# Kernel optimization log

Hardware: AMD Instinct MI355X
Metric: run time of the kernel (lower is better)

Reference implementation:

```python
import math
import jax, jax.numpy as jnp
import numpy as np

SQRT_2_OVER_PI = 0.7978845608028654
FACIL_RATE = 2.0
FIRE_THRESH = 0.88
EPS = 1e-05

def _gelu(x):
    return 0.5 * x * (1.0 + jnp.tanh(SQRT_2_OVER_PI * (x + 0.044715 * x ** 3)))

def setup_inputs() -> dict:
    key = jax.random.key(0)
    ks = jax.random.split(key, 8)
    B, T, D, N = 4, 4096, 1024, 512
    x = jax.random.normal(ks[0], (B, T, D), jnp.float32)
    ema_x = jax.random.normal(ks[1], (D,), jnp.float32) * 0.1
    ema_x2 = ema_x ** 2 + jax.random.uniform(ks[2], (D,), jnp.float32) + 0.5
    ema_y = jax.random.normal(ks[3], (D,), jnp.float32) * 0.1
    ema_y2 = ema_y ** 2 + jax.random.uniform(ks[4], (D,), jnp.float32) + 0.5
    buf = jax.random.normal(ks[5], (N, D), jnp.float32)
    buf = buf / jnp.linalg.norm(buf, axis=-1, keepdims=True)
    facil = 1.0 + 2.0 * jax.random.uniform(ks[6], (N,), jnp.float32)  # facilitation levels >= 1
    mask = jnp.ones((N,), dtype=bool)
    return {
        'x': x,
        'log_tau_in': jnp.float32(math.log(1.0)),
        'log_tau_out': jnp.float32(math.log(1.0)),
        'log_a_in': jnp.float32(0.0),
        'log_a_out': jnp.float32(0.0),
        'log_k_boost': jnp.float32(math.log(0.5)),
        'log_k_damp': jnp.float32(math.log(0.3)),
        'ema_x': ema_x, 'ema_x2': ema_x2, 'ema_y': ema_y, 'ema_y2': ema_y2,
        'buf': buf, 'facil': facil, 'mask': mask,
    }

def reference(x, log_tau_in, log_tau_out, log_a_in, log_a_out,
              log_k_boost, log_k_damp, ema_x, ema_x2, ema_y, ema_y2,
              buf, facil, mask):
    sg = jax.lax.stop_gradient
    D = x.shape[-1]
    y = _gelu(x)
    # --- gate_211 (l1_ready steady state); z-statistics are detached in torch ---
    tau_in, tau_out = jnp.exp(log_tau_in), jnp.exp(log_tau_out)
    a_in, a_out = jax.nn.sigmoid(log_a_in), jax.nn.sigmoid(log_a_out)
    std_x = jnp.sqrt(jnp.clip(sg(ema_x2) - sg(ema_x) ** 2, 0.0)) + EPS
    z_in = jnp.mean(((sg(x) - sg(ema_x)) / std_x) ** 2, axis=-1)        # [B,T]
    std_y = jnp.sqrt(jnp.clip(sg(ema_y2) - sg(ema_y) ** 2, 0.0)) + EPS
    z_out = jnp.mean(((sg(y) - sg(ema_y)) / std_y) ** 2, axis=-1)       # [B,T]
    g_in = 1.0 - a_in + a_in * jnp.exp(-tau_in * z_in)
    g_out = 1.0 - a_out + a_out * jnp.exp(-tau_out * z_out)
    gate = g_in * g_out
    y1 = y * gate[..., None]
    # --- eval-time OCS nearest-neighbor facilitation (l2_ready, pass1_complete) ---
    k_boost = jnp.clip(jnp.exp(log_k_boost), 0.01, 4.0)
    k_damp = jnp.clip(jnp.exp(log_k_damp), 0.01, 0.9)
    y1_mean = jnp.mean(sg(y1).reshape(-1, D), axis=0)                    # [D]
    m_n = y1_mean / jnp.maximum(jnp.linalg.norm(y1_mean), 1e-12)
    buf_sg = sg(buf)
    buf_n = buf_sg / jnp.maximum(jnp.linalg.norm(buf_sg, axis=-1, keepdims=True), 1e-12)
    sims = jnp.where(mask, buf_n @ m_n, -1.0)                            # [N]
    nearest_idx = jnp.argmax(sims)
    sim_val = jnp.clip(sims[nearest_idx], 0.0, 1.0)
    fired = sim_val > FIRE_THRESH
    facil_level = sg(facil)[nearest_idx] * jnp.where(fired, FACIL_RATE, 1.0)
    v = buf_sg[nearest_idx]                                              # [D]
    valid = jnp.all(jnp.isfinite(v)) & (jnp.linalg.norm(v) >= 1e-06)
    mod = (facil_level - 1.0) * sim_val
    boost = 1.0 + sg(k_boost) * mod            # torch uses .item(): detached
    damp = jnp.maximum(0.01, 1.0 - sg(k_damp) * mod)
    proj = jnp.sum(y1 * v, axis=-1, keepdims=True)
    y_par = proj * v
    out = jnp.where(valid, y_par * boost + (y1 - y_par) * damp, y1)
    return out
```

## Files before the change

kernel.cpp:

```cpp
#include <hip/hip_runtime.h>
#include <math.h>

#define D 1024
#define NROWS 16384
#define NBUF 512
#define NBLKA 512
#define NSLOT 512

#define OFF_MEAN 0
#define OFF_KEY  1024
#define OFF_GATE 2048
#define OFF_PART 20480
#define ZERO_BYTES 4112

typedef float nfloat4 __attribute__((ext_vector_type(4)));

__device__ __forceinline__ float4 ld4(const float* p) { return *(const float4*)p; }
__device__ __forceinline__ void st4_nt(float* p, float4 v) {
    nfloat4 nv = { v.x, v.y, v.z, v.w };
    __builtin_nontemporal_store(nv, (nfloat4*)p);
}

__device__ __forceinline__ float wave_red(float v) {
    #pragma unroll
    for (int off = 32; off > 0; off >>= 1) v += __shfl_xor(v, off, 64);
    return v;
}

__device__ __forceinline__ float gelu_f(float x) {
    float x2 = x * x;
    float t1 = fmaf(0.044715f, x2, 1.0f);
    float u2 = (1.5957691216057308f * x) * t1;
    float e  = __expf(u2);
    float r  = __builtin_amdgcn_rcpf(e + 1.0f);
    return fmaf(-x, r, x);
}

__device__ __forceinline__ float4 gelu4(float4 x) {
    float4 y;
    y.x = gelu_f(x.x); y.y = gelu_f(x.y); y.z = gelu_f(x.z); y.w = gelu_f(x.w);
    return y;
}

#define LOADPAIR(rr, XA, XB) do {                                              \
    const float* _pA = x + (size_t)(rr) * D;                                   \
    const float* _pB = _pA + D;                                                \
    _Pragma("unroll")                                                          \
    for (int _j = 0; _j < 4; ++_j) {                                           \
        XA[_j] = ld4(&_pA[col[_j]]);                                           \
        XB[_j] = ld4(&_pB[col[_j]]);                                           \
    }                                                                          \
} while (0)

__global__ __launch_bounds__(256, 2) void k_passA(const float* __restrict__ x,
                                                  const float* __restrict__ ema_x,
                                                  const float* __restrict__ ema_x2,
                                                  const float* __restrict__ ema_y,
                                                  const float* __restrict__ ema_y2,
                                                  const float* __restrict__ lti,
                                                  const float* __restrict__ lto,
                                                  const float* __restrict__ lai,
                                                  const float* __restrict__ lao,
                                                  float* __restrict__ ws) {
    __shared__ float s_stat[4096];
    __shared__ float s_acc[D];
    const int tid = threadIdx.x, wave = tid >> 6, lane = tid & 63;

    for (int i = tid; i < 1024; i += 256) {
        float mx = ema_x[i];
        float vx = fmaxf(ema_x2[i] - mx * mx, 0.0f);
        float ax = 1.0f / (sqrtf(vx) + 1e-5f);
        s_stat[i]        = ax;
        s_stat[1024 + i] = mx * ax;
        float my = ema_y[i];
        float vy = fmaxf(ema_y2[i] - my * my, 0.0f);
        float ay = 1.0f / (sqrtf(vy) + 1e-5f);
        s_stat[2048 + i] = ay;
        s_stat[3072 + i] = my * ay;
        s_acc[i] = 0.0f;
    }
    __syncthreads();

    const float tau_in = __expf(lti[0]), tau_out = __expf(lto[0]);
    const float a_in  = 1.0f / (1.0f + __expf(-lai[0]));
    const float a_out = 1.0f / (1.0f + __expf(-lao[0]));

    int col[4];
    #pragma unroll
    for (int j = 0; j < 4; ++j) col[j] = 4 * lane + 256 * j;

    float4 acc[4];
    #pragma unroll
    for (int j = 0; j < 4; ++j) acc[j] = make_float4(0.f, 0.f, 0.f, 0.f);

#define COMPPAIR_A(rr, XA, XB) do {                                            \
    float4 yA[4], yB[4];                                                       \
    float zinA = 0.f, zinB = 0.f, zoutA = 0.f, zoutB = 0.f;                    \
    _Pragma("unroll")                                                          \
    for (int j = 0; j < 4; ++j) {                                              \
        float4 a  = *(const float4*)&s_stat[col[j]];                           \
        float4 bb = *(const float4*)&s_stat[1024 + col[j]];                    \
        float d;                                                               \
        d = fmaf(XA[j].x, a.x, -bb.x); zinA = fmaf(d, d, zinA);                \
        d = fmaf(XA[j].y, a.y, -bb.y); zinA = fmaf(d, d, zinA);                \
        d = fmaf(XA[j].z, a.z, -bb.z); zinA = fmaf(d, d, zinA);                \
        d = fmaf(XA[j].w, a.w, -bb.w); zinA = fmaf(d, d, zinA);                \
        d = fmaf(XB[j].x, a.x, -bb.x); zinB = fmaf(d, d, zinB);                \
        d = fmaf(XB[j].y, a.y, -bb.y); zinB = fmaf(d, d, zinB);                \
        d = fmaf(XB[j].z, a.z, -bb.z); zinB = fmaf(d, d, zinB);                \
        d = fmaf(XB[j].w, a.w, -bb.w); zinB = fmaf(d, d, zinB);                \
        yA[j] = gelu4(XA[j]);                                                  \
        yB[j] = gelu4(XB[j]);                                                  \
        float4 ay = *(const float4*)&s_stat[2048 + col[j]];                    \
        float4 by = *(const float4*)&s_stat[3072 + col[j]];                    \
        d = fmaf(yA[j].x, ay.x, -by.x); zoutA = fmaf(d, d, zoutA);             \
        d = fmaf(yA[j].y, ay.y, -by.y); zoutA = fmaf(d, d, zoutA);             \
        d = fmaf(yA[j].z, ay.z, -by.z); zoutA = fmaf(d, d, zoutA);             \
        d = fmaf(yA[j].w, ay.w, -by.w); zoutA = fmaf(d, d, zoutA);             \
        d = fmaf(yB[j].x, ay.x, -by.x); zoutB = fmaf(d, d, zoutB);             \
        d = fmaf(yB[j].y, ay.y, -by.y); zoutB = fmaf(d, d, zoutB);             \
        d = fmaf(yB[j].z, ay.z, -by.z); zoutB = fmaf(d, d, zoutB);             \
        d = fmaf(yB[j].w, ay.w, -by.w); zoutB = fmaf(d, d, zoutB);             \
    }                                                                          \
    zinA  = wave_red(zinA)  * (1.0f / D);                                      \
    zinB  = wave_red(zinB)  * (1.0f / D);                                      \
    zoutA = wave_red(zoutA) * (1.0f / D);                                      \
    zoutB = wave_red(zoutB) * (1.0f / D);                                      \
    float gA = ((1.0f - a_in)  + a_in  * __expf(-tau_in  * zinA)) *            \
               ((1.0f - a_out) + a_out * __expf(-tau_out * zoutA));            \
    float gB = ((1.0f - a_in)  + a_in  * __expf(-tau_in  * zinB)) *            \
               ((1.0f - a_out) + a_out * __expf(-tau_out * zoutB));            \
    if (lane == 0) { ws[OFF_GATE + (rr)] = gA; ws[OFF_GATE + (rr) + 1] = gB; } \
    _Pragma("unroll")                                                          \
    for (int j = 0; j < 4; ++j) {                                              \
        acc[j].x = fmaf(yA[j].x, gA, fmaf(yB[j].x, gB, acc[j].x));             \
        acc[j].y = fmaf(yA[j].y, gA, fmaf(yB[j].y, gB, acc[j].y));             \
        acc[j].z = fmaf(yA[j].z, gA, fmaf(yB[j].z, gB, acc[j].z));             \
        acc[j].w = fmaf(yA[j].w, gA, fmaf(yB[j].w, gB, acc[j].w));             \
    }                                                                          \
} while (0)

    const int r0 = (blockIdx.x * 4 + wave) * 8;
    float4 xA0[4], xB0[4], xA1[4], xB1[4];

    LOADPAIR(r0 + 0, xA0, xB0);
    LOADPAIR(r0 + 2, xA1, xB1);
    COMPPAIR_A(r0 + 0, xA0, xB0);
    LOADPAIR(r0 + 4, xA0, xB0);
    COMPPAIR_A(r0 + 2, xA1, xB1);
    LOADPAIR(r0 + 6, xA1, xB1);
    COMPPAIR_A(r0 + 4, xA0, xB0);
    COMPPAIR_A(r0 + 6, xA1, xB1);

    #pragma unroll
    for (int j = 0; j < 4; ++j) {
        atomicAdd(&s_acc[col[j] + 0], acc[j].x);
        atomicAdd(&s_acc[col[j] + 1], acc[j].y);
        atomicAdd(&s_acc[col[j] + 2], acc[j].z);
        atomicAdd(&s_acc[col[j] + 3], acc[j].w);
    }
    __syncthreads();
    *(float4*)&ws[OFF_PART + (size_t)blockIdx.x * D + 4 * tid] = *(float4*)&s_acc[4 * tid];
}

__global__ __launch_bounds__(256) void k_mean(float* __restrict__ ws) {
    const int tid = threadIdx.x;
    const float* P = &ws[OFF_PART + (size_t)blockIdx.x * 16 * D];
    float4 s = make_float4(0.f, 0.f, 0.f, 0.f);
    #pragma unroll
    for (int i = 0; i < 16; ++i) {
        float4 v = ld4(&P[(size_t)i * D + 4 * tid]);
        s.x += v.x; s.y += v.y; s.z += v.z; s.w += v.w;
    }
    atomicAdd(&ws[OFF_MEAN + 4 * tid + 0], s.x);
    atomicAdd(&ws[OFF_MEAN + 4 * tid + 1], s.y);
    atomicAdd(&ws[OFF_MEAN + 4 * tid + 2], s.z);
    atomicAdd(&ws[OFF_MEAN + 4 * tid + 3], s.w);
}

__global__ __launch_bounds__(256) void k_sims(const float* __restrict__ buf,
                                              const unsigned char* __restrict__ mask,
                                              float* __restrict__ ws) {
    __shared__ float s_red[4];
    __shared__ float s_inv;
    const int tid = threadIdx.x, wave = tid >> 6, lane = tid & 63;

    float4 mv = ld4(&ws[OFF_MEAN + 4 * tid]);
    float ns = mv.x * mv.x + mv.y * mv.y + mv.z * mv.z + mv.w * mv.w;
    ns = wave_red(ns);
    if (lane == 0) s_red[wave] = ns;
    __syncthreads();
    if (tid == 0) {
        float t = s_red[0] + s_red[1] + s_red[2] + s_red[3];
        s_inv = 1.0f / fmaxf(sqrtf(t), 1e-12f);
    }
    __syncthreads();
    const float inv = s_inv;

    int col[4];
    float4 mvv[4];
    #pragma unroll
    for (int j = 0; j < 4; ++j) {
        col[j] = 4 * lane + 256 * j;
        mvv[j] = ld4(&ws[OFF_MEAN + col[j]]);
    }
    const int n = blockIdx.x * 4 + wave;
    const float* br = buf + (size_t)n * D;
    float dot = 0.f, bns = 0.f;
    #pragma unroll
    for (int j = 0; j < 4; ++j) {
        float4 bv = ld4(&br[col[j]]);
        dot = fmaf(bv.x, mvv[j].x, dot); dot = fmaf(bv.y, mvv[j].y, dot);
        dot = fmaf(bv.z, mvv[j].z, dot); dot = fmaf(bv.w, mvv[j].w, dot);
        bns = fmaf(bv.x, bv.x, bns); bns = fmaf(bv.y, bv.y, bns);
        bns = fmaf(bv.z, bv.z, bns); bns = fmaf(bv.w, bv.w, bns);
    }
    dot = wave_red(dot);
    bns = wave_red(bns);
    if (lane == 0) {
        float sim = -1.0f;
        if (mask[n]) sim = (dot * inv) / fmaxf(sqrtf(bns), 1e-12f);
        unsigned int fb = __float_as_uint(sim);
        unsigned int mono = (fb & 0x80000000u) ? ~fb : (fb | 0x80000000u);
        unsigned long long key = ((unsigned long long)mono << 32) | (unsigned int)(~n);
        atomicMax((unsigned long long*)&ws[OFF_KEY], key);
    }
}

__global__ __launch_bounds__(256, 2) void k_passB(const float* __restrict__ x,
                                                  const float* __restrict__ buf,
                                                  const float* __restrict__ facil,
                                                  const float* __restrict__ lkb,
                                                  const float* __restrict__ lkd,
                                                  const float* __restrict__ ws,
                                                  float* __restrict__ out) {
    __shared__ float s_v[D];
    __shared__ float s_red[4];
    __shared__ float s_sc[3];
    const int tid = threadIdx.x, wave = tid >> 6, lane = tid & 63;

    const unsigned long long key = *(const unsigned long long*)&ws[OFF_KEY];
    const int idx = (int)(~(unsigned int)(key & 0xFFFFFFFFull));
    const unsigned int mono = (unsigned int)(key >> 32);
    const unsigned int fb = (mono & 0x80000000u) ? (mono ^ 0x80000000u) : ~mono;
    const float sim = __uint_as_float(fb);

    float4 vt = ld4(&buf[(size_t)idx * D + 4 * tid]);
    float bns = 0.f;
    if (!isfinite(vt.x) || !isfinite(vt.y) || !isfinite(vt.z) || !isfinite(vt.w))
        bns = __uint_as_float(0x7FC00000u);
    bns += vt.x * vt.x + vt.y * vt.y + vt.z * vt.z + vt.w * vt.w;
    bns = wave_red(bns);
    if (lane == 0) s_red[wave] = bns;
    __syncthreads();
    if (tid == 0) {
        float t = s_red[0] + s_red[1] + s_red[2] + s_red[3];
        int valid = (t >= 1e-12f) ? 1 : 0;
        float sim_val = fminf(fmaxf(sim, 0.0f), 1.0f);
        float fl = facil[idx] * ((sim_val > 0.88f) ? 2.0f : 1.0f);
        float mod = (fl - 1.0f) * sim_val;
        float kb = fminf(fmaxf(__expf(lkb[0]), 0.01f), 4.0f);
        float kd = fminf(fmaxf(__expf(lkd[0]), 0.01f), 0.9f);
        float boost = 1.0f + kb * mod;
        float damp = fmaxf(0.01f, 1.0f - kd * mod);
        s_sc[0] = valid ? damp : 1.0f;
        s_sc[1] = valid ? (boost - damp) : 0.0f;
        s_sc[2] = (float)valid;
    }
    __syncthreads();
    const float dampe = s_sc[0], coef = s_sc[1];
    if (s_sc[2] == 0.0f) vt = make_float4(0.f, 0.f, 0.f, 0.f);
    *(float4*)&s_v[4 * tid] = vt;
    __syncthreads();

    int col[4];
    float4 vv[4];
    #pragma unroll
    for (int j = 0; j < 4; ++j) {
        col[j] = 4 * lane + 256 * j;
        vv[j] = *(const float4*)&s_v[col[j]];
    }

#define COMPPAIR_B(rr, XA, XB) do {                                            \
    const float gA = ws[OFF_GATE + (rr)], gB = ws[OFF_GATE + (rr) + 1];        \
    float4 yA[4], yB[4];                                                       \
    float projA = 0.f, projB = 0.f;                                            \
    _Pragma("unroll")                                                          \
    for (int j = 0; j < 4; ++j) {                                              \
        yA[j] = gelu4(XA[j]);                                                  \
        yA[j].x *= gA; yA[j].y *= gA; yA[j].z *= gA; yA[j].w *= gA;            \
        yB[j] = gelu4(XB[j]);                                                  \
        yB[j].x *= gB; yB[j].y *= gB; yB[j].z *= gB; yB[j].w *= gB;            \
        projA = fmaf(yA[j].x, vv[j].x, projA); projA = fmaf(yA[j].y, vv[j].y, projA); \
        projA = fmaf(yA[j].z, vv[j].z, projA); projA = fmaf(yA[j].w, vv[j].w, projA); \
        projB = fmaf(yB[j].x, vv[j].x, projB); projB = fmaf(yB[j].y, vv[j].y, projB); \
        projB = fmaf(yB[j].z, vv[j].z, projB); projB = fmaf(yB[j].w, vv[j].w, projB); \
    }                                                                          \
    projA = wave_red(projA);                                                   \
    projB = wave_red(projB);                                                   \
    const float pcA = projA * coef, pcB = projB * coef;                        \
    float* oA = out + (size_t)(rr) * D;                                        \
    float* oB = oA + D;                                                        \
    _Pragma("unroll")                                                          \
    for (int j = 0; j < 4; ++j) {                                              \
        float4 o;                                                              \
        o.x = fmaf(yA[j].x, dampe, pcA * vv[j].x);                             \
        o.y = fmaf(yA[j].y, dampe, pcA * vv[j].y);                             \
        o.z = fmaf(yA[j].z, dampe, pcA * vv[j].z);                             \
        o.w = fmaf(yA[j].w, dampe, pcA * vv[j].w);                             \
        st4_nt(&oA[col[j]], o);                                                \
        o.x = fmaf(yB[j].x, dampe, pcB * vv[j].x);                             \
        o.y = fmaf(yB[j].y, dampe, pcB * vv[j].y);                             \
        o.z = fmaf(yB[j].z, dampe, pcB * vv[j].z);                             \
        o.w = fmaf(yB[j].w, dampe, pcB * vv[j].w);                             \
        st4_nt(&oB[col[j]], o);                                                \
    }                                                                          \
} while (0)

    const int r0 = (blockIdx.x * 4 + wave) * 8;
    float4 xA0[4], xB0[4], xA1[4], xB1[4];

    LOADPAIR(r0 + 0, xA0, xB0);
    LOADPAIR(r0 + 2, xA1, xB1);
    COMPPAIR_B(r0 + 0, xA0, xB0);
    LOADPAIR(r0 + 4, xA0, xB0);
    COMPPAIR_B(r0 + 2, xA1, xB1);
    LOADPAIR(r0 + 6, xA1, xB1);
    COMPPAIR_B(r0 + 4, xA0, xB0);
    COMPPAIR_B(r0 + 6, xA1, xB1);
}

extern "C" void kernel_launch(void* const* d_in, const int* in_sizes, int n_in,
                              void* d_out, int out_size, void* d_ws, size_t ws_size,
                              hipStream_t stream) {
    const float* x      = (const float*)d_in[0];
    const float* lti    = (const float*)d_in[1];
    const float* lto    = (const float*)d_in[2];
    const float* lai    = (const float*)d_in[3];
    const float* lao    = (const float*)d_in[4];
    const float* lkb    = (const float*)d_in[5];
    const float* lkd    = (const float*)d_in[6];
    const float* ema_x  = (const float*)d_in[7];
    const float* ema_x2 = (const float*)d_in[8];
    const float* ema_y  = (const float*)d_in[9];
    const float* ema_y2 = (const float*)d_in[10];
    const float* buf    = (const float*)d_in[11];
    const float* facil  = (const float*)d_in[12];
    const unsigned char* mask = (const unsigned char*)d_in[13];
    float* ws  = (float*)d_ws;
    float* out = (float*)d_out;

    (void)hipMemsetAsync(d_ws, 0, ZERO_BYTES, stream);
    hipLaunchKernelGGL(k_passA, dim3(NBLKA), dim3(256), 0, stream,
                       x, ema_x, ema_x2, ema_y, ema_y2, lti, lto, lai, lao, ws);
    hipLaunchKernelGGL(k_mean,  dim3(NSLOT / 16), dim3(256), 0, stream, ws);
    hipLaunchKernelGGL(k_sims,  dim3(128), dim3(256), 0, stream, buf, mask, ws);
    hipLaunchKernelGGL(k_passB, dim3(NBLKA), dim3(256), 0, stream,
                       x, buf, facil, lkb, lkd, ws, out);
}
```

Measured before the change: 176.5 us.

## Fuse all passes into one cooperative kernel keeping gated activations in registers

```diff
diff --git a/kernel.cpp b/kernel.cpp
--- a/kernel.cpp
+++ b/kernel.cpp
@@ -1,10 +1,13 @@
 #include <hip/hip_runtime.h>
+#include <hip/hip_cooperative_groups.h>
 #include <math.h>
+
+namespace cg = cooperative_groups;
 
 #define D 1024
 #define NROWS 16384
 #define NBUF 512
-#define NBLKA 512
+#define NBLK 512
 #define NSLOT 512
 
 #define OFF_MEAN 0
@@ -51,6 +54,247 @@
         XB[_j] = ld4(&_pB[col[_j]]);                                           \
     }                                                                          \
 } while (0)
+
+__global__ __launch_bounds__(256, 2) void k_fused(
+    const float* __restrict__ x,
+    const float* __restrict__ ema_x,  const float* __restrict__ ema_x2,
+    const float* __restrict__ ema_y,  const float* __restrict__ ema_y2,
+    const float* __restrict__ lti,    const float* __restrict__ lto,
+    const float* __restrict__ lai,    const float* __restrict__ lao,
+    const float* __restrict__ lkb,    const float* __restrict__ lkd,
+    const float* __restrict__ buf,    const float* __restrict__ facil,
+    const unsigned char* __restrict__ mask,
+    float* __restrict__ ws,           float* __restrict__ out)
+{
+    cg::grid_group grid = cg::this_grid();
+    __shared__ float s_stat[4096];
+    __shared__ float s_acc[D];
+    __shared__ float s_red[4];
+    __shared__ float s_sc[3];
+    __shared__ float s_inv;
+    const int tid = threadIdx.x, wave = tid >> 6, lane = tid & 63;
+
+    for (int i = tid; i < 1024; i += 256) {
+        float mx = ema_x[i];
+        float vx = fmaxf(ema_x2[i] - mx * mx, 0.0f);
+        float ax = 1.0f / (sqrtf(vx) + 1e-5f);
+        s_stat[i]        = ax;
+        s_stat[1024 + i] = mx * ax;
+        float my = ema_y[i];
+        float vy = fmaxf(ema_y2[i] - my * my, 0.0f);
+        float ay = 1.0f / (sqrtf(vy) + 1e-5f);
+        s_stat[2048 + i] = ay;
+        s_stat[3072 + i] = my * ay;
+        s_acc[i] = 0.0f;
+    }
+    __syncthreads();
+
+    const float tau_in = __expf(lti[0]), tau_out = __expf(lto[0]);
+    const float a_in  = 1.0f / (1.0f + __expf(-lai[0]));
+    const float a_out = 1.0f / (1.0f + __expf(-lao[0]));
+
+    int col[4];
+    #pragma unroll
+    for (int j = 0; j < 4; ++j) col[j] = 4 * lane + 256 * j;
+
+    float4 acc[4];
+    #pragma unroll
+    for (int j = 0; j < 4; ++j) acc[j] = make_float4(0.f, 0.f, 0.f, 0.f);
+
+#define COMPPAIR_F(XA, XB, YA, YB) do {                                        \
+    float zinA = 0.f, zinB = 0.f, zoutA = 0.f, zoutB = 0.f;                    \
+    _Pragma("unroll")                                                          \
+    for (int j = 0; j < 4; ++j) {                                              \
+        float4 a  = *(const float4*)&s_stat[col[j]];                           \
+        float4 bb = *(const float4*)&s_stat[1024 + col[j]];                    \
+        float d;                                                               \
+        d = fmaf(XA[j].x, a.x, -bb.x); zinA = fmaf(d, d, zinA);                \
+        d = fmaf(XA[j].y, a.y, -bb.y); zinA = fmaf(d, d, zinA);                \
+        d = fmaf(XA[j].z, a.z, -bb.z); zinA = fmaf(d, d, zinA);                \
+        d = fmaf(XA[j].w, a.w, -bb.w); zinA = fmaf(d, d, zinA);                \
+        d = fmaf(XB[j].x, a.x, -bb.x); zinB = fmaf(d, d, zinB);                \
+        d = fmaf(XB[j].y, a.y, -bb.y); zinB = fmaf(d, d, zinB);                \
+        d = fmaf(XB[j].z, a.z, -bb.z); zinB = fmaf(d, d, zinB);                \
+        d = fmaf(XB[j].w, a.w, -bb.w); zinB = fmaf(d, d, zinB);                \
+        YA[j] = gelu4(XA[j]);                                                  \
+        YB[j] = gelu4(XB[j]);                                                  \
+        float4 ay = *(const float4*)&s_stat[2048 + col[j]];                    \
+        float4 by = *(const float4*)&s_stat[3072 + col[j]];                    \
+        d = fmaf(YA[j].x, ay.x, -by.x); zoutA = fmaf(d, d, zoutA);             \
+        d = fmaf(YA[j].y, ay.y, -by.y); zoutA = fmaf(d, d, zoutA);             \
+        d = fmaf(YA[j].z, ay.z, -by.z); zoutA = fmaf(d, d, zoutA);             \
+        d = fmaf(YA[j].w, ay.w, -by.w); zoutA = fmaf(d, d, zoutA);             \
+        d = fmaf(YB[j].x, ay.x, -by.x); zoutB = fmaf(d, d, zoutB);             \
+        d = fmaf(YB[j].y, ay.y, -by.y); zoutB = fmaf(d, d, zoutB);             \
+        d = fmaf(YB[j].z, ay.z, -by.z); zoutB = fmaf(d, d, zoutB);             \
+        d = fmaf(YB[j].w, ay.w, -by.w); zoutB = fmaf(d, d, zoutB);             \
+    }                                                                          \
+    zinA  = wave_red(zinA)  * (1.0f / D);                                      \
+    zinB  = wave_red(zinB)  * (1.0f / D);                                      \
+    zoutA = wave_red(zoutA) * (1.0f / D);                                      \
+    zoutB = wave_red(zoutB) * (1.0f / D);                                      \
+    float gA = ((1.0f - a_in)  + a_in  * __expf(-tau_in  * zinA)) *            \
+               ((1.0f - a_out) + a_out * __expf(-tau_out * zoutA));            \
+    float gB = ((1.0f - a_in)  + a_in  * __expf(-tau_in  * zinB)) *            \
+               ((1.0f - a_out) + a_out * __expf(-tau_out * zoutB));            \
+    _Pragma("unroll")                                                          \
+    for (int j = 0; j < 4; ++j) {                                              \
+        YA[j].x *= gA; YA[j].y *= gA; YA[j].z *= gA; YA[j].w *= gA;            \
+        YB[j].x *= gB; YB[j].y *= gB; YB[j].z *= gB; YB[j].w *= gB;            \
+        acc[j].x += YA[j].x + YB[j].x;                                         \
+        acc[j].y += YA[j].y + YB[j].y;                                         \
+        acc[j].z += YA[j].z + YB[j].z;                                         \
+        acc[j].w += YA[j].w + YB[j].w;                                         \
+    }                                                                          \
+} while (0)
+
+    const int r0 = (blockIdx.x * 4 + wave) * 8;
+    float4 xA0[4], xB0[4], xA1[4], xB1[4];
+    float4 y0A[4], y0B[4], y1A[4], y1B[4], y2A[4], y2B[4], y3A[4], y3B[4];
+
+    LOADPAIR(r0 + 0, xA0, xB0);
+    LOADPAIR(r0 + 2, xA1, xB1);
+    COMPPAIR_F(xA0, xB0, y0A, y0B);
+    LOADPAIR(r0 + 4, xA0, xB0);
+    COMPPAIR_F(xA1, xB1, y1A, y1B);
+    LOADPAIR(r0 + 6, xA1, xB1);
+    COMPPAIR_F(xA0, xB0, y2A, y2B);
+    COMPPAIR_F(xA1, xB1, y3A, y3B);
+#undef COMPPAIR_F
+
+    #pragma unroll
+    for (int j = 0; j < 4; ++j) {
+        atomicAdd(&s_acc[col[j] + 0], acc[j].x);
+        atomicAdd(&s_acc[col[j] + 1], acc[j].y);
+        atomicAdd(&s_acc[col[j] + 2], acc[j].z);
+        atomicAdd(&s_acc[col[j] + 3], acc[j].w);
+    }
+    __syncthreads();
+    {
+        float4 a4 = *(float4*)&s_acc[4 * tid];
+        atomicAdd(&ws[OFF_MEAN + 4 * tid + 0], a4.x);
+        atomicAdd(&ws[OFF_MEAN + 4 * tid + 1], a4.y);
+        atomicAdd(&ws[OFF_MEAN + 4 * tid + 2], a4.z);
+        atomicAdd(&ws[OFF_MEAN + 4 * tid + 3], a4.w);
+    }
+
+    grid.sync();
+
+    if (blockIdx.x < NBUF / 4) {
+        float4 mv = ld4(&ws[OFF_MEAN + 4 * tid]);
+        float ns = mv.x * mv.x + mv.y * mv.y + mv.z * mv.z + mv.w * mv.w;
+        ns = wave_red(ns);
+        if (lane == 0) s_red[wave] = ns;
+        __syncthreads();
+        if (tid == 0) {
+            float t = s_red[0] + s_red[1] + s_red[2] + s_red[3];
+            s_inv = 1.0f / fmaxf(sqrtf(t), 1e-12f);
+        }
+        __syncthreads();
+        const float inv = s_inv;
+
+        float4 mvv[4];
+        #pragma unroll
+        for (int j = 0; j < 4; ++j) mvv[j] = ld4(&ws[OFF_MEAN + col[j]]);
+        const int n = blockIdx.x * 4 + wave;
+        const float* br = buf + (size_t)n * D;
+        float dot = 0.f, bns = 0.f;
+        #pragma unroll
+        for (int j = 0; j < 4; ++j) {
+            float4 bv = ld4(&br[col[j]]);
+            dot = fmaf(bv.x, mvv[j].x, dot); dot = fmaf(bv.y, mvv[j].y, dot);
+            dot = fmaf(bv.z, mvv[j].z, dot); dot = fmaf(bv.w, mvv[j].w, dot);
+            bns = fmaf(bv.x, bv.x, bns); bns = fmaf(bv.y, bv.y, bns);
+            bns = fmaf(bv.z, bv.z, bns); bns = fmaf(bv.w, bv.w, bns);
+        }
+        dot = wave_red(dot);
+        bns = wave_red(bns);
+        if (lane == 0) {
+            float sim = -1.0f;
+            if (mask[n]) sim = (dot * inv) / fmaxf(sqrtf(bns), 1e-12f);
+            unsigned int fb = __float_as_uint(sim);
+            unsigned int mono = (fb & 0x80000000u) ? ~fb : (fb | 0x80000000u);
+            unsigned long long key = ((unsigned long long)mono << 32) | (unsigned int)(~n);
+            atomicMax((unsigned long long*)&ws[OFF_KEY], key);
+        }
+    }
+
+    grid.sync();
+
+    const unsigned long long key = *(const unsigned long long*)&ws[OFF_KEY];
+    const int idx = (int)(~(unsigned int)(key & 0xFFFFFFFFull));
+    const unsigned int mono = (unsigned int)(key >> 32);
+    const unsigned int fb = (mono & 0x80000000u) ? (mono ^ 0x80000000u) : ~mono;
+    const float sim = __uint_as_float(fb);
+
+    float4 vt = ld4(&buf[(size_t)idx * D + 4 * tid]);
+    float bns = 0.f;
+    if (!isfinite(vt.x) || !isfinite(vt.y) || !isfinite(vt.z) || !isfinite(vt.w))
+        bns = __uint_as_float(0x7FC00000u);
+    bns += vt.x * vt.x + vt.y * vt.y + vt.z * vt.z + vt.w * vt.w;
+    bns = wave_red(bns);
+    if (lane == 0) s_red[wave] = bns;
+    __syncthreads();
+    if (tid == 0) {
+        float t = s_red[0] + s_red[1] + s_red[2] + s_red[3];
+        int valid = (t >= 1e-12f) ? 1 : 0;
+        float sim_val = fminf(fmaxf(sim, 0.0f), 1.0f);
+        float fl = facil[idx] * ((sim_val > 0.88f) ? 2.0f : 1.0f);
+        float mod = (fl - 1.0f) * sim_val;
+        float kb = fminf(fmaxf(__expf(lkb[0]), 0.01f), 4.0f);
+        float kd = fminf(fmaxf(__expf(lkd[0]), 0.01f), 0.9f);
+        float boost = 1.0f + kb * mod;
+        float damp = fmaxf(0.01f, 1.0f - kd * mod);
+        s_sc[0] = valid ? damp : 1.0f;
+        s_sc[1] = valid ? (boost - damp) : 0.0f;
+        s_sc[2] = (float)valid;
+    }
+    __syncthreads();
+    const float dampe = s_sc[0], coef = s_sc[1];
+    if (s_sc[2] == 0.0f) vt = make_float4(0.f, 0.f, 0.f, 0.f);
+    *(float4*)&s_acc[4 * tid] = vt;
+    __syncthreads();
+
+    float4 vv[4];
+    #pragma unroll
+    for (int j = 0; j < 4; ++j) vv[j] = *(const float4*)&s_acc[col[j]];
+
+#define OUTPAIR(rr, YA, YB) do {                                               \
+    float projA = 0.f, projB = 0.f;                                            \
+    _Pragma("unroll")                                                          \
+    for (int j = 0; j < 4; ++j) {                                              \
+        projA = fmaf(YA[j].x, vv[j].x, projA); projA = fmaf(YA[j].y, vv[j].y, projA); \
+        projA = fmaf(YA[j].z, vv[j].z, projA); projA = fmaf(YA[j].w, vv[j].w, projA); \
+        projB = fmaf(YB[j].x, vv[j].x, projB); projB = fmaf(YB[j].y, vv[j].y, projB); \
+        projB = fmaf(YB[j].z, vv[j].z, projB); projB = fmaf(YB[j].w, vv[j].w, projB); \
+    }                                                                          \
+    projA = wave_red(projA);                                                   \
+    projB = wave_red(projB);                                                   \
+    const float pcA = projA * coef, pcB = projB * coef;                        \
+    float* oA = out + (size_t)(rr) * D;                                        \
+    float* oB = oA + D;                                                        \
+    _Pragma("unroll")                                                          \
+    for (int j = 0; j < 4; ++j) {                                              \
+        float4 o;                                                              \
+        o.x = fmaf(YA[j].x, dampe, pcA * vv[j].x);                             \
+        o.y = fmaf(YA[j].y, dampe, pcA * vv[j].y);                             \
+        o.z = fmaf(YA[j].z, dampe, pcA * vv[j].z);                             \
+        o.w = fmaf(YA[j].w, dampe, pcA * vv[j].w);                             \
+        st4_nt(&oA[col[j]], o);                                                \
+        o.x = fmaf(YB[j].x, dampe, pcB * vv[j].x);                             \
+        o.y = fmaf(YB[j].y, dampe, pcB * vv[j].y);                             \
+        o.z = fmaf(YB[j].z, dampe, pcB * vv[j].z);                             \
+        o.w = fmaf(YB[j].w, dampe, pcB * vv[j].w);                             \
+        st4_nt(&oB[col[j]], o);                                                \
+    }                                                                          \
+} while (0)
+
+    OUTPAIR(r0 + 0, y0A, y0B);
+    OUTPAIR(r0 + 2, y1A, y1B);
+    OUTPAIR(r0 + 4, y2A, y2B);
+    OUTPAIR(r0 + 6, y3A, y3B);
+#undef OUTPAIR
+}
 
 __global__ __launch_bounds__(256, 2) void k_passA(const float* __restrict__ x,
                                                   const float* __restrict__ ema_x,
@@ -151,6 +395,7 @@
     LOADPAIR(r0 + 6, xA1, xB1);
     COMPPAIR_A(r0 + 4, xA0, xB0);
     COMPPAIR_A(r0 + 6, xA1, xB1);
+#undef COMPPAIR_A
 
     #pragma unroll
     for (int j = 0; j < 4; ++j) {
@@ -328,6 +573,7 @@
     LOADPAIR(r0 + 6, xA1, xB1);
     COMPPAIR_B(r0 + 4, xA0, xB0);
     COMPPAIR_B(r0 + 6, xA1, xB1);
+#undef COMPPAIR_B
 }
 
 extern "C" void kernel_launch(void* const* d_in, const int* in_sizes, int n_in,
@@ -351,10 +597,20 @@
     float* out = (float*)d_out;
 
     (void)hipMemsetAsync(d_ws, 0, ZERO_BYTES, stream);
-    hipLaunchKernelGGL(k_passA, dim3(NBLKA), dim3(256), 0, stream,
-                       x, ema_x, ema_x2, ema_y, ema_y2, lti, lto, lai, lao, ws);
-    hipLaunchKernelGGL(k_mean,  dim3(NSLOT / 16), dim3(256), 0, stream, ws);
-    hipLaunchKernelGGL(k_sims,  dim3(128), dim3(256), 0, stream, buf, mask, ws);
-    hipLaunchKernelGGL(k_passB, dim3(NBLKA), dim3(256), 0, stream,
-                       x, buf, facil, lkb, lkd, ws, out);
-}
+
+    void* args[] = { (void*)&x, (void*)&ema_x, (void*)&ema_x2, (void*)&ema_y,
+                     (void*)&ema_y2, (void*)&lti, (void*)&lto, (void*)&lai,
+                     (void*)&lao, (void*)&lkb, (void*)&lkd, (void*)&buf,
+                     (void*)&facil, (void*)&mask, (void*)&ws, (void*)&out };
+    hipError_t ce = hipLaunchCooperativeKernel((const void*)k_fused,
+                                               dim3(NBLK), dim3(256),
+                                               args, 0, stream);
+    if (ce != hipSuccess) {
+        hipLaunchKernelGGL(k_passA, dim3(NBLK), dim3(256), 0, stream,
+                           x, ema_x, ema_x2, ema_y, ema_y2, lti, lto, lai, lao, ws);
+        hipLaunchKernelGGL(k_mean,  dim3(NSLOT / 16), dim3(256), 0, stream, ws);
+        hipLaunchKernelGGL(k_sims,  dim3(128), dim3(256), 0, stream, buf, mask, ws);
+        hipLaunchKernelGGL(k_passB, dim3(NBLK), dim3(256), 0, stream,
+                           x, buf, facil, lkb, lkd, ws, out);
+    }
+}
```

Result: slower. 304.4 us (+72.5%).
